# Performance work log

Measured on AMD Instinct MI355X. Metric: run time of the kernel, lower is better.

The kernel has to match this reference:

```python
import jax, jax.numpy as jnp
import numpy as np

N_IN, M_MID = 512, 256
B, H, W = 16, 64, 64

def setup_inputs() -> dict:
    key = jax.random.key(0)
    ks = jax.random.split(key, 7)
    s = 0.05
    return {
        "x": jax.random.normal(ks[0], (B, N_IN, H, W), dtype=jnp.float32),
        "W_state": jax.random.normal(ks[1], (M_MID, N_IN), dtype=jnp.float32) * s,
        "b_state": jax.random.normal(ks[2], (M_MID,), dtype=jnp.float32) * s,
        "W_proj": jax.random.normal(ks[3], (M_MID, N_IN), dtype=jnp.float32) * s,
        "b_proj": jax.random.normal(ks[4], (M_MID,), dtype=jnp.float32) * s,
        "W_extend": jax.random.normal(ks[5], (N_IN, M_MID), dtype=jnp.float32) * s,
        "b_extend": jax.random.normal(ks[6], (N_IN,), dtype=jnp.float32) * s,
    }

def reference(x, W_state, b_state, W_proj, b_proj, W_extend, b_extend):
    n, c, h, w = x.shape
    hw = h * w
    xf = x.reshape(n, c, hw)                                   # [n, C, HW]
    # 1x1 convs are channel GEMMs over flattened spatial dim
    x_state = jnp.einsum('mc,nch->nmh', W_state, xf) + b_state[None, :, None]   # [n, M, HW]
    x_proj = jnp.einsum('mc,nch->nmh', W_proj, xf) + b_proj[None, :, None]      # [n, M, HW]
    # bmm -> scale -> softmax -> bmm (graph reasoning over M x M)
    scores = jnp.einsum('nmh,nkh->nmk', x_state, x_proj) / jnp.sqrt(jnp.float32(hw))
    attn = jax.nn.softmax(scores, axis=2)                      # [n, M, M]
    x_rstate = jnp.einsum('nmk,nkh->nmh', attn, x_proj)        # [n, M, HW]
    # extend back to C channels + residual
    ext = jnp.einsum('cm,nmh->nch', W_extend, x_rstate) + b_extend[None, :, None]
    return x + ext.reshape(n, c, h, w)
```

## Files before the change

kernel.cpp:

```cpp
#include <hip/hip_runtime.h>
#include <hip/hip_bf16.h>
#include <stdint.h>

typedef __bf16 bf16x8_t __attribute__((ext_vector_type(8)));
typedef float  f32x4_t  __attribute__((ext_vector_type(4)));
typedef short  short8_t __attribute__((ext_vector_type(8)));

__device__ __forceinline__ unsigned short f2b(float f) {
    union { float f; unsigned u; } v; v.f = f;
    unsigned u = v.u;
    return (unsigned short)((u + 0x7FFFu + ((u >> 16) & 1u)) >> 16);
}

#define AS3(p) ((__attribute__((address_space(3))) void*)(p))
#define AS1(p) ((const __attribute__((address_space(1))) void*)(p))
#define FENCE() asm volatile("" ::: "memory")

#define NB   16
#define CIN  512
#define MMID 256
#define HW   4096
#define KSPLIT 8
#define ASZ  (128 * 64)

__device__ __forceinline__ void swz3(int gx, int gy, int& bx, int& by, int& bz) {
    const int nwg = gridDim.x, ord = blockIdx.x, q = nwg >> 3;
    const int s = (ord & 7) * q + (ord >> 3);
    bx = s % gx;
    const int rem = s / gx;
    by = rem % gy;
    bz = rem / gy;
}

__global__ __launch_bounds__(256) void prep_weights(
    const float* __restrict__ Ws, const float* __restrict__ Wp,
    const float* __restrict__ Wef, const float* __restrict__ bs,
    const float* __restrict__ bp,
    unsigned short* __restrict__ Wsp, unsigned short* __restrict__ Wex,
    float* __restrict__ bsp)
{
    int i = blockIdx.x * 256 + threadIdx.x;
    if (i < MMID * CIN) {
        Wsp[i]              = f2b(Ws[i]);
        Wsp[MMID * CIN + i] = f2b(Wp[i]);
        Wex[i]              = f2b(Wef[i]);
    }
    if (i < MMID) { bsp[i] = bs[i]; bsp[MMID + i] = bp[i]; }
}

__global__ __launch_bounds__(256) void transpose_convert_x(
    const float* __restrict__ x, unsigned short* __restrict__ xT)
{
    __shared__ unsigned short tile[64][66];
    const int n = blockIdx.z, c0 = blockIdx.y * 64, h0 = blockIdx.x * 64;
    const float* s = x + ((size_t)n * CIN + c0) * HW + h0;
    unsigned short* d = xT + ((size_t)n * HW + h0) * CIN + c0;
    const int t = threadIdx.x;
    {
        const int rr = t >> 4, cc = (t & 15) * 4;
        #pragma unroll
        for (int p = 0; p < 4; ++p) {
            int r = p * 16 + rr;
            float4 v = *(const float4*)(s + (size_t)r * HW + cc);
            tile[r][cc + 0] = f2b(v.x); tile[r][cc + 1] = f2b(v.y);
            tile[r][cc + 2] = f2b(v.z); tile[r][cc + 3] = f2b(v.w);
        }
    }
    __syncthreads();
    {
        const int wr = t >> 3, wc = (t & 7) * 8;
        #pragma unroll
        for (int p = 0; p < 2; ++p) {
            int h = p * 32 + wr;
            unsigned short tmp[8];
            #pragma unroll
            for (int j = 0; j < 8; ++j) tmp[j] = tile[wc + j][h];
            *(short8_t*)(d + (size_t)h * CIN + wc) = *(const short8_t*)tmp;
        }
    }
}

__global__ __launch_bounds__(256) void transpose_bf16_64(
    const unsigned short* __restrict__ src, unsigned short* __restrict__ dst,
    int srs, int drs, long long sbs, long long dbs)
{
    __shared__ unsigned short tile[64][66];
    const int n = blockIdx.z, r0 = blockIdx.y * 64, c0 = blockIdx.x * 64;
    const unsigned short* s = src + (size_t)n * sbs + (size_t)r0 * srs + c0;
    unsigned short* d = dst + (size_t)n * dbs + (size_t)c0 * drs + r0;
    const int t = threadIdx.x;
    const int rr = t >> 3, cc = (t & 7) * 8;
    #pragma unroll
    for (int p = 0; p < 2; ++p) {
        int r = p * 32 + rr;
        short8_t v = *(const short8_t*)(s + (size_t)r * srs + cc);
        #pragma unroll
        for (int j = 0; j < 8; ++j) tile[r][cc + j] = ((const unsigned short*)&v)[j];
    }
    __syncthreads();
    #pragma unroll
    for (int p = 0; p < 2; ++p) {
        int c = p * 32 + rr;
        unsigned short tmp[8];
        #pragma unroll
        for (int j = 0; j < 8; ++j) tmp[j] = tile[cc + j][c];
        *(short8_t*)(d + (size_t)c * drs + cc) = *(const short8_t*)tmp;
    }
}

template <int EPI>
__device__ __forceinline__ void epilogue_repack(
    f32x4_t (&acc)[4][4], unsigned short* smem,
    int m0, int n0, int wave, int lane,
    const float* __restrict__ bias, const float* __restrict__ resid,
    void* __restrict__ Cout, int ldc, size_t cbase)
{
    float* fbuf = (float*)smem;
    const int t   = wave * 64 + lane;
    const int l15 = lane & 15, l16 = lane >> 4;
    const int wr2 = wave >> 1;
    const int wc  = (wave & 1) * 64;

    #pragma unroll
    for (int p = 0; p < 4; ++p) {
        __syncthreads();
        if (wr2 == (p >> 1)) {
            const int ihalf = p & 1;
            #pragma unroll
            for (int i2 = 0; i2 < 2; ++i2) {
                const int i = ihalf * 2 + i2;
                #pragma unroll
                for (int r = 0; r < 4; ++r) {
                    const int lrow = i2 * 16 + l16 * 4 + r;
                    #pragma unroll
                    for (int j = 0; j < 4; ++j)
                        fbuf[lrow * 132 + wc + j * 16 + l15] = acc[i][j][r];
                }
            }
        }
        __syncthreads();
        #pragma unroll
        for (int it = 0; it < 2; ++it) {
            const int lrow = it * 16 + (t >> 4);
            const int col  = (t & 15) * 8;
            const int row  = m0 + p * 32 + lrow;
            float v[8];
            *(float4*)&v[0] = *(const float4*)&fbuf[lrow * 132 + col];
            *(float4*)&v[4] = *(const float4*)&fbuf[lrow * 132 + col + 4];
            float badd = 0.f;
            if constexpr (EPI == 0 || EPI == 3) badd = bias[row];
            const size_t idx = cbase + (size_t)row * ldc + n0 + col;
            if constexpr (EPI == 3) {
                float o[8];
                const float* rp = resid + idx;
                float4 r0 = *(const float4*)rp;
                float4 r1 = *(const float4*)(rp + 4);
                o[0] = v[0] + badd + r0.x; o[1] = v[1] + badd + r0.y;
                o[2] = v[2] + badd + r0.z; o[3] = v[3] + badd + r0.w;
                o[4] = v[4] + badd + r1.x; o[5] = v[5] + badd + r1.y;
                o[6] = v[6] + badd + r1.z; o[7] = v[7] + badd + r1.w;
                float* op = (float*)Cout + idx;
                *(float4*)op = *(const float4*)&o[0];
                *(float4*)(op + 4) = *(const float4*)&o[4];
            } else if constexpr (EPI == 1) {
                float* op = (float*)Cout + idx;
                *(float4*)op = *(const float4*)&v[0];
                *(float4*)(op + 4) = *(const float4*)&v[4];
            } else {
                unsigned short o[8];
                #pragma unroll
                for (int k = 0; k < 8; ++k) o[k] = f2b(v[k] + badd);
                *(short8_t*)((unsigned short*)Cout + idx) = *(const short8_t*)o;
            }
        }
    }
}

#define GEMM_KLOOP(Ab, Bb, lda, ldb, KBEG, NT)                                          \
    auto stage = [&](int k0, int b) {                                                   \
        unsigned short* Asb = smem + b * 2 * ASZ;                                       \
        unsigned short* Bsb = Asb + ASZ;                                                \
        _Pragma("unroll")                                                               \
        for (int c = 0; c < 4; ++c) {                                                   \
            const int o   = (c * 256 + t) * 16;                                         \
            const int row = o >> 7;                                                     \
            const int ce  = ((o & 127) ^ ((row & 7) << 4)) >> 1;                        \
            __builtin_amdgcn_global_load_lds(                                           \
                AS1(Ab + (size_t)row * lda + k0 + ce), AS3((char*)Asb + o), 16, 0, 0);  \
            __builtin_amdgcn_global_load_lds(                                           \
                AS1(Bb + (size_t)row * ldb + k0 + ce), AS3((char*)Bsb + o), 16, 0, 0);  \
        }                                                                               \
    };                                                                                  \
    stage(KBEG, 0);                                                                     \
    for (int itk = 0; itk < (NT); ++itk) {                                              \
        const int cur = itk & 1;                                                        \
        if (itk + 1 < (NT)) {                                                           \
            stage(KBEG + (itk + 1) * 64, cur ^ 1);                                      \
            asm volatile("s_waitcnt vmcnt(8)" ::: "memory");                            \
        } else {                                                                        \
            asm volatile("s_waitcnt vmcnt(0)" ::: "memory");                            \
        }                                                                               \
        __builtin_amdgcn_s_barrier();                                                   \
        FENCE();                                                                        \
        const char* Asb = (const char*)(smem + cur * 2 * ASZ);                          \
        const char* Bsb = Asb + 2 * ASZ;                                                \
        const int swz = (l15 & 7) << 4;                                                 \
        _Pragma("unroll")                                                               \
        for (int ks = 0; ks < 2; ++ks) {                                                \
            bf16x8_t af[4], bfr[4];                                                     \
            const int cb = (ks * 64 + l16 * 16) ^ swz;                                  \
            _Pragma("unroll")                                                           \
            for (int i = 0; i < 4; ++i) {                                               \
                af[i]  = *(const bf16x8_t*)(Asb + (wr + i * 16 + l15) * 128 + cb);      \
                bfr[i] = *(const bf16x8_t*)(Bsb + (wc + i * 16 + l15) * 128 + cb);      \
            }                                                                           \
            _Pragma("unroll")                                                           \
            for (int i = 0; i < 4; ++i)                                                 \
                _Pragma("unroll")                                                       \
                for (int j = 0; j < 4; ++j)                                             \
                    acc[i][j] = __builtin_amdgcn_mfma_f32_16x16x32_bf16(                \
                        af[i], bfr[j], acc[i][j], 0, 0, 0);                             \
        }                                                                               \
        FENCE();                                                                        \
        __builtin_amdgcn_s_barrier();                                                   \
        FENCE();                                                                        \
    }

__global__ __launch_bounds__(256) void gemm_conv(
    const unsigned short* __restrict__ Wsp, const unsigned short* __restrict__ xT,
    const float* __restrict__ bsp,
    unsigned short* __restrict__ Ysp, unsigned short* __restrict__ xprojT)
{
    __shared__ unsigned short smem[4 * ASZ];

    int bx, by, n;  swz3(HW / 128, CIN / 128, bx, by, n);
    const int m0 = by * 128;
    const int h0 = bx * 128;

    const unsigned short* Ab = Wsp + (size_t)m0 * CIN;
    const unsigned short* Bb = xT + (size_t)n * HW * CIN + (size_t)h0 * CIN;

    const int t    = threadIdx.x;
    const int lane = t & 63;
    const int wave = t >> 6;
    const int wr   = (wave >> 1) * 64;
    const int wc   = (wave & 1) * 64;
    const int l15  = lane & 15;
    const int l16  = lane >> 4;

    f32x4_t acc[4][4] = {};
    GEMM_KLOOP(Ab, Bb, CIN, CIN, 0, CIN / 64)

    float* fbuf = (float*)smem;
    const int wr2 = wave >> 1;
    unsigned short* Yb = Ysp + (size_t)n * CIN * HW;
    #pragma unroll
    for (int p = 0; p < 4; ++p) {
        __syncthreads();
        if (wr2 == (p >> 1)) {
            const int ihalf = p & 1;
            #pragma unroll
            for (int i2 = 0; i2 < 2; ++i2) {
                const int i = ihalf * 2 + i2;
                #pragma unroll
                for (int r = 0; r < 4; ++r) {
                    const int lrow = i2 * 16 + l16 * 4 + r;
                    #pragma unroll
                    for (int j = 0; j < 4; ++j)
                        fbuf[lrow * 132 + wc + j * 16 + l15] = acc[i][j][r];
                }
            }
        }
        __syncthreads();
        #pragma unroll
        for (int it = 0; it < 2; ++it) {
            const int lrow = it * 16 + (t >> 4);
            const int col  = (t & 15) * 8;
            const int row  = m0 + p * 32 + lrow;
            const float badd = bsp[row];
            float v[8];
            *(float4*)&v[0] = *(const float4*)&fbuf[lrow * 132 + col];
            *(float4*)&v[4] = *(const float4*)&fbuf[lrow * 132 + col + 4];
            unsigned short o8[8];
            #pragma unroll
            for (int k = 0; k < 8; ++k) o8[k] = f2b(v[k] + badd);
            *(short8_t*)(Yb + (size_t)row * HW + h0 + col) = *(const short8_t*)o8;
        }
        if (m0 >= MMID) {
            const int h = t >> 1, ksub = (t & 1) * 16;
            unsigned short o16[16];
            #pragma unroll
            for (int i = 0; i < 16; ++i) {
                const int lr = ksub + i;
                o16[i] = f2b(fbuf[lr * 132 + h] + bsp[m0 + p * 32 + lr]);
            }
            unsigned short* dp = xprojT + ((size_t)n * HW + h0 + h) * MMID
                                 + (m0 - MMID) + p * 32 + ksub;
            *(short8_t*)dp       = *(const short8_t*)&o16[0];
            *(short8_t*)(dp + 8) = *(const short8_t*)&o16[8];
        }
    }
}

__global__ __launch_bounds__(256) void gemm_scores(
    const unsigned short* __restrict__ Ysp, float* __restrict__ scoresP)
{
    __shared__ unsigned short smem[4 * ASZ];

    int bx, by, z;  swz3(MMID / 128, MMID / 128, bx, by, z);
    const int n  = z >> 3;
    const int kc = z & 7;
    const int m0 = by * 128;
    const int n0 = bx * 128;

    const unsigned short* Ab = Ysp + (size_t)n * CIN * HW + (size_t)m0 * HW;
    const unsigned short* Bb = Ysp + (size_t)n * CIN * HW + (size_t)(MMID + n0) * HW;

    const int t    = threadIdx.x;
    const int lane = t & 63;
    const int wave = t >> 6;
    const int wr   = (wave >> 1) * 64;
    const int wc   = (wave & 1) * 64;
    const int l15  = lane & 15;
    const int l16  = lane >> 4;

    f32x4_t acc[4][4] = {};
    const int kbeg = kc * (HW / KSPLIT);
    GEMM_KLOOP(Ab, Bb, HW, HW, kbeg, (HW / KSPLIT) / 64)

    float* outp = scoresP + (size_t)(kc * NB + n) * MMID * MMID;
    epilogue_repack<1>(acc, smem, m0, n0, wave, lane, nullptr, nullptr,
                       outp, MMID, 0);
}

__global__ __launch_bounds__(256) void softmax_rows(
    const float* __restrict__ scoresP, unsigned short* __restrict__ attn)
{
    const int wave = threadIdx.x >> 6;
    const int l    = threadIdx.x & 63;
    const size_t row = (size_t)blockIdx.x * 4 + wave;
    const size_t pstride = (size_t)NB * MMID * MMID;
    float4 v = {0.f, 0.f, 0.f, 0.f};
    #pragma unroll
    for (int p = 0; p < KSPLIT; ++p) {
        float4 u = *(const float4*)(scoresP + p * pstride + row * MMID + l * 4);
        v.x += u.x; v.y += u.y; v.z += u.z; v.w += u.w;
    }
    float mx = fmaxf(fmaxf(v.x, v.y), fmaxf(v.z, v.w));
    #pragma unroll
    for (int off = 32; off; off >>= 1) mx = fmaxf(mx, __shfl_xor(mx, off));
    const float sc = 0.015625f;
    float e0 = __expf((v.x - mx) * sc), e1 = __expf((v.y - mx) * sc);
    float e2 = __expf((v.z - mx) * sc), e3 = __expf((v.w - mx) * sc);
    float sum = e0 + e1 + e2 + e3;
    #pragma unroll
    for (int off = 32; off; off >>= 1) sum += __shfl_xor(sum, off);
    const float inv = 1.0f / sum;
    unsigned short o[4] = { f2b(e0 * inv), f2b(e1 * inv), f2b(e2 * inv), f2b(e3 * inv) };
    *(uint64_t*)(attn + row * MMID + l * 4) = *(const uint64_t*)o;
}

template <int EPI>
__global__ __launch_bounds__(256) void gemm_nt(
    const unsigned short* __restrict__ A, const unsigned short* __restrict__ B,
    int lda, int ldb, int K,
    long long strideA, long long strideB,
    const float* __restrict__ bias,
    const float* __restrict__ resid,
    void* __restrict__ Cout, int ldc, long long strideC,
    int gx, int gy)
{
    __shared__ unsigned short smem[4 * ASZ];

    int bx, by, n;  swz3(gx, gy, bx, by, n);
    const int m0 = by * 128;
    const int n0 = bx * 128;

    const unsigned short* Ab = A + (size_t)n * strideA + (size_t)m0 * lda;
    const unsigned short* Bb = B + (size_t)n * strideB + (size_t)n0 * ldb;

    const int t    = threadIdx.x;
    const int lane = t & 63;
    const int wave = t >> 6;
    const int wr   = (wave >> 1) * 64;
    const int wc   = (wave & 1) * 64;
    const int l15  = lane & 15;
    const int l16  = lane >> 4;

    f32x4_t acc[4][4] = {};
    GEMM_KLOOP(Ab, Bb, lda, ldb, 0, K / 64)

    epilogue_repack<EPI>(acc, smem, m0, n0, wave, lane, bias, resid,
                         Cout, ldc, (size_t)n * strideC);
}

extern "C" void kernel_launch(void* const* d_in, const int* in_sizes, int n_in,
                              void* d_out, int out_size, void* d_ws, size_t ws_size,
                              hipStream_t stream)
{
    const float* x   = (const float*)d_in[0];
    const float* Ws  = (const float*)d_in[1];
    const float* bs  = (const float*)d_in[2];
    const float* Wp  = (const float*)d_in[3];
    const float* bp  = (const float*)d_in[4];
    const float* Wef = (const float*)d_in[5];
    const float* be  = (const float*)d_in[6];
    float* out = (float*)d_out;

    unsigned short* xT     = (unsigned short*)d_ws;
    unsigned short* Ysp    = xT     + (size_t)NB * HW * CIN;
    unsigned short* xprojT = Ysp    + (size_t)NB * CIN * HW;
    unsigned short* Wsp    = xprojT + (size_t)NB * HW * MMID;
    unsigned short* Wex    = Wsp    + (size_t)CIN * CIN;
    unsigned short* attn   = Wex    + (size_t)CIN * MMID;
    unsigned short* attnT  = attn   + (size_t)NB * MMID * MMID;
    unsigned short* G      = attnT  + (size_t)NB * MMID * MMID;
    float* bsp = (float*)(G + (size_t)NB * CIN * MMID);
    float* scoresP = (float*)xT;

    prep_weights<<<512, 256, 0, stream>>>(Ws, Wp, Wef, bs, bp, Wsp, Wex, bsp);

    transpose_convert_x<<<dim3(HW / 64, CIN / 64, NB), 256, 0, stream>>>(x, xT);

    gemm_conv<<<(HW / 128) * (CIN / 128) * NB, 256, 0, stream>>>(
        Wsp, xT, bsp, Ysp, xprojT);

    gemm_scores<<<(MMID / 128) * (MMID / 128) * NB * KSPLIT, 256, 0, stream>>>(
        Ysp, scoresP);

    softmax_rows<<<NB * MMID / 4, 256, 0, stream>>>(scoresP, attn);

    transpose_bf16_64<<<dim3(MMID / 64, MMID / 64, NB), 256, 0, stream>>>(
        attn, attnT, MMID, MMID, (long long)MMID * MMID, (long long)MMID * MMID);

    gemm_nt<2><<<(MMID / 128) * (CIN / 128) * NB, 256, 0, stream>>>(
        Wex, attnT, MMID, MMID, MMID,
        0LL, (long long)MMID * MMID,
        nullptr, nullptr, G, MMID, (long long)CIN * MMID,
        MMID / 128, CIN / 128);

    gemm_nt<3><<<(HW / 128) * (CIN / 128) * NB, 256, 0, stream>>>(
        G, xprojT, MMID, MMID, MMID,
        (long long)CIN * MMID, (long long)HW * MMID,
        be, x, out, HW, (long long)CIN * HW,
        HW / 128, CIN / 128);
}
```

Before: 203.7 us.

## Fold projection weights into extend GEMM to skip xproj transpose

The final GEMM now uses a fused per-batch matrix Meff = G·W_proj (512x512) applied directly to the transposed input, and the projection bias is folded into a per-batch bias vector. This lets the conv GEMM drop its transposed x_proj side write and use the shared epilogue. The cost is that the last GEMM's K dimension doubles from 256 to 512, which adds FLOPs, and two small extra kernels (compute_vec and the Meff GEMM) are launched. The block swizzle order is also changed.

```diff
diff --git a/kernel.cpp b/kernel.cpp
--- a/kernel.cpp
+++ b/kernel.cpp
@@ -10,6 +10,9 @@
     union { float f; unsigned u; } v; v.f = f;
     unsigned u = v.u;
     return (unsigned short)((u + 0x7FFFu + ((u >> 16) & 1u)) >> 16);
+}
+__device__ __forceinline__ float b2f(unsigned short b) {
+    union { unsigned u; float f; } v; v.u = ((unsigned)b) << 16; return v.f;
 }
 
 #define AS3(p) ((__attribute__((address_space(3))) void*)(p))
@@ -26,10 +29,10 @@
 __device__ __forceinline__ void swz3(int gx, int gy, int& bx, int& by, int& bz) {
     const int nwg = gridDim.x, ord = blockIdx.x, q = nwg >> 3;
     const int s = (ord & 7) * q + (ord >> 3);
-    bx = s % gx;
-    const int rem = s / gx;
-    by = rem % gy;
-    bz = rem / gy;
+    by = s % gy;
+    const int rem = s / gy;
+    bx = rem % gx;
+    bz = rem / gx;
 }
 
 __global__ __launch_bounds__(256) void prep_weights(
@@ -37,13 +40,15 @@
     const float* __restrict__ Wef, const float* __restrict__ bs,
     const float* __restrict__ bp,
     unsigned short* __restrict__ Wsp, unsigned short* __restrict__ Wex,
-    float* __restrict__ bsp)
+    unsigned short* __restrict__ WpT, float* __restrict__ bsp)
 {
     int i = blockIdx.x * 256 + threadIdx.x;
     if (i < MMID * CIN) {
         Wsp[i]              = f2b(Ws[i]);
         Wsp[MMID * CIN + i] = f2b(Wp[i]);
         Wex[i]              = f2b(Wef[i]);
+        const int c = i >> 8, k = i & (MMID - 1);
+        WpT[i] = f2b(Wp[(size_t)k * CIN + c]);
     }
     if (i < MMID) { bsp[i] = bs[i]; bsp[MMID + i] = bp[i]; }
 }
@@ -228,8 +233,7 @@
 
 __global__ __launch_bounds__(256) void gemm_conv(
     const unsigned short* __restrict__ Wsp, const unsigned short* __restrict__ xT,
-    const float* __restrict__ bsp,
-    unsigned short* __restrict__ Ysp, unsigned short* __restrict__ xprojT)
+    const float* __restrict__ bsp, unsigned short* __restrict__ Ysp)
 {
     __shared__ unsigned short smem[4 * ASZ];
 
@@ -251,55 +255,8 @@
     f32x4_t acc[4][4] = {};
     GEMM_KLOOP(Ab, Bb, CIN, CIN, 0, CIN / 64)
 
-    float* fbuf = (float*)smem;
-    const int wr2 = wave >> 1;
-    unsigned short* Yb = Ysp + (size_t)n * CIN * HW;
-    #pragma unroll
-    for (int p = 0; p < 4; ++p) {
-        __syncthreads();
-        if (wr2 == (p >> 1)) {
-            const int ihalf = p & 1;
-            #pragma unroll
-            for (int i2 = 0; i2 < 2; ++i2) {
-                const int i = ihalf * 2 + i2;
-                #pragma unroll
-                for (int r = 0; r < 4; ++r) {
-                    const int lrow = i2 * 16 + l16 * 4 + r;
-                    #pragma unroll
-                    for (int j = 0; j < 4; ++j)
-                        fbuf[lrow * 132 + wc + j * 16 + l15] = acc[i][j][r];
-                }
-            }
-        }
-        __syncthreads();
-        #pragma unroll
-        for (int it = 0; it < 2; ++it) {
-            const int lrow = it * 16 + (t >> 4);
-            const int col  = (t & 15) * 8;
-            const int row  = m0 + p * 32 + lrow;
-            const float badd = bsp[row];
-            float v[8];
-            *(float4*)&v[0] = *(const float4*)&fbuf[lrow * 132 + col];
-            *(float4*)&v[4] = *(const float4*)&fbuf[lrow * 132 + col + 4];
-            unsigned short o8[8];
-            #pragma unroll
-            for (int k = 0; k < 8; ++k) o8[k] = f2b(v[k] + badd);
-            *(short8_t*)(Yb + (size_t)row * HW + h0 + col) = *(const short8_t*)o8;
-        }
-        if (m0 >= MMID) {
-            const int h = t >> 1, ksub = (t & 1) * 16;
-            unsigned short o16[16];
-            #pragma unroll
-            for (int i = 0; i < 16; ++i) {
-                const int lr = ksub + i;
-                o16[i] = f2b(fbuf[lr * 132 + h] + bsp[m0 + p * 32 + lr]);
-            }
-            unsigned short* dp = xprojT + ((size_t)n * HW + h0 + h) * MMID
-                                 + (m0 - MMID) + p * 32 + ksub;
-            *(short8_t*)dp       = *(const short8_t*)&o16[0];
-            *(short8_t*)(dp + 8) = *(const short8_t*)&o16[8];
-        }
-    }
+    epilogue_repack<0>(acc, smem, m0, h0, wave, lane, bsp, nullptr,
+                       Ysp, HW, (size_t)n * CIN * HW);
 }
 
 __global__ __launch_bounds__(256) void gemm_scores(
@@ -360,12 +317,29 @@
     *(uint64_t*)(attn + row * MMID + l * 4) = *(const uint64_t*)o;
 }
 
+__global__ __launch_bounds__(256) void compute_vec(
+    const unsigned short* __restrict__ G, const float* __restrict__ bsp,
+    const float* __restrict__ be, float* __restrict__ vec)
+{
+    const int n = blockIdx.x >> 1;
+    const int c = ((blockIdx.x & 1) << 8) + threadIdx.x;
+    const unsigned short* g = G + ((size_t)n * CIN + c) * MMID;
+    float s = 0.f;
+    for (int k = 0; k < MMID; k += 8) {
+        short8_t v = *(const short8_t*)(g + k);
+        #pragma unroll
+        for (int j = 0; j < 8; ++j)
+            s += b2f((unsigned short)v[j]) * bsp[MMID + k + j];
+    }
+    vec[n * CIN + c] = be[c] + s;
+}
+
 template <int EPI>
 __global__ __launch_bounds__(256) void gemm_nt(
     const unsigned short* __restrict__ A, const unsigned short* __restrict__ B,
     int lda, int ldb, int K,
     long long strideA, long long strideB,
-    const float* __restrict__ bias,
+    const float* __restrict__ bias, int bias_bstride,
     const float* __restrict__ resid,
     void* __restrict__ Cout, int ldc, long long strideC,
     int gx, int gy)
@@ -390,7 +364,8 @@
     f32x4_t acc[4][4] = {};
     GEMM_KLOOP(Ab, Bb, lda, ldb, 0, K / 64)
 
-    epilogue_repack<EPI>(acc, smem, m0, n0, wave, lane, bias, resid,
+    const float* beff = bias ? bias + (size_t)n * bias_bstride : nullptr;
+    epilogue_repack<EPI>(acc, smem, m0, n0, wave, lane, beff, resid,
                          Cout, ldc, (size_t)n * strideC);
 }
 
@@ -407,23 +382,25 @@
     const float* be  = (const float*)d_in[6];
     float* out = (float*)d_out;
 
-    unsigned short* xT     = (unsigned short*)d_ws;
-    unsigned short* Ysp    = xT     + (size_t)NB * HW * CIN;
-    unsigned short* xprojT = Ysp    + (size_t)NB * CIN * HW;
-    unsigned short* Wsp    = xprojT + (size_t)NB * HW * MMID;
-    unsigned short* Wex    = Wsp    + (size_t)CIN * CIN;
-    unsigned short* attn   = Wex    + (size_t)CIN * MMID;
-    unsigned short* attnT  = attn   + (size_t)NB * MMID * MMID;
-    unsigned short* G      = attnT  + (size_t)NB * MMID * MMID;
-    float* bsp = (float*)(G + (size_t)NB * CIN * MMID);
-    float* scoresP = (float*)xT;
-
-    prep_weights<<<512, 256, 0, stream>>>(Ws, Wp, Wef, bs, bp, Wsp, Wex, bsp);
+    unsigned short* xT   = (unsigned short*)d_ws;
+    unsigned short* Ysp  = xT   + (size_t)NB * HW * CIN;
+    unsigned short* Wsp  = Ysp  + (size_t)NB * CIN * HW;
+    unsigned short* Wex  = Wsp  + (size_t)CIN * CIN;
+    unsigned short* WpT  = Wex  + (size_t)CIN * MMID;
+    unsigned short* attn = WpT  + (size_t)CIN * MMID;
+    unsigned short* attnT= attn + (size_t)NB * MMID * MMID;
+    unsigned short* G    = attnT+ (size_t)NB * MMID * MMID;
+    unsigned short* Meff = G    + (size_t)NB * CIN * MMID;
+    float* scoresP = (float*)(Meff + (size_t)NB * CIN * CIN);
+    float* bsp = scoresP + (size_t)KSPLIT * NB * MMID * MMID;
+    float* vec = bsp + CIN;
+
+    prep_weights<<<512, 256, 0, stream>>>(Ws, Wp, Wef, bs, bp, Wsp, Wex, WpT, bsp);
 
     transpose_convert_x<<<dim3(HW / 64, CIN / 64, NB), 256, 0, stream>>>(x, xT);
 
     gemm_conv<<<(HW / 128) * (CIN / 128) * NB, 256, 0, stream>>>(
-        Wsp, xT, bsp, Ysp, xprojT);
+        Wsp, xT, bsp, Ysp);
 
     gemm_scores<<<(MMID / 128) * (MMID / 128) * NB * KSPLIT, 256, 0, stream>>>(
         Ysp, scoresP);
@@ -436,12 +413,20 @@
     gemm_nt<2><<<(MMID / 128) * (CIN / 128) * NB, 256, 0, stream>>>(
         Wex, attnT, MMID, MMID, MMID,
         0LL, (long long)MMID * MMID,
-        nullptr, nullptr, G, MMID, (long long)CIN * MMID,
+        nullptr, 0, nullptr, G, MMID, (long long)CIN * MMID,
         MMID / 128, CIN / 128);
 
+    compute_vec<<<NB * 2, 256, 0, stream>>>(G, bsp, be, vec);
+
+    gemm_nt<2><<<(CIN / 128) * (CIN / 128) * NB, 256, 0, stream>>>(
+        G, WpT, MMID, MMID, MMID,
+        (long long)CIN * MMID, 0LL,
+        nullptr, 0, nullptr, Meff, CIN, (long long)CIN * CIN,
+        CIN / 128, CIN / 128);
+
     gemm_nt<3><<<(HW / 128) * (CIN / 128) * NB, 256, 0, stream>>>(
-        G, xprojT, MMID, MMID, MMID,
-        (long long)CIN * MMID, (long long)HW * MMID,
-        be, x, out, HW, (long long)CIN * HW,
+        Meff, xT, CIN, CIN, CIN,
+        (long long)CIN * CIN, (long long)HW * CIN,
+        vec, CIN, x, out, HW, (long long)CIN * HW,
         HW / 128, CIN / 128);
 }
```

Result: slower. 217.3 us (+6.7%).
